# Kernel optimization log

Hardware: AMD Instinct MI355X
Metric: run time of the kernel (lower is better)

Reference implementation:

```python
import jax, jax.numpy as jnp
import numpy as np

H = 1024       # hidden_size
NH = 16        # num_heads
HD = H // NH   # head_dim
I = 4096       # intermediate_size
EPS = 1e-6


def setup_inputs() -> dict:
    key = jax.random.key(0)
    ks = jax.random.split(key, 10)
    s = 0.02
    return {
        "hidden_states": jax.random.normal(ks[0], (8, 1025, H), jnp.float32),
        "qkv_w": jax.random.normal(ks[1], (3 * H, H), jnp.float32) * s,
        "qkv_b": jnp.zeros((3 * H,), jnp.float32),
        "proj_w": jax.random.normal(ks[2], (H, H), jnp.float32) * s,
        "proj_b": jnp.zeros((H,), jnp.float32),
        "fc1_w": jax.random.normal(ks[3], (I, H), jnp.float32) * s,
        "fc1_b": jnp.zeros((I,), jnp.float32),
        "fc2_w": jax.random.normal(ks[4], (H, I), jnp.float32) * s,
        "fc2_b": jnp.zeros((H,), jnp.float32),
        "norm1_w": jnp.ones((H,), jnp.float32),
        "norm1_b": jnp.zeros((H,), jnp.float32),
        "norm2_w": jnp.ones((H,), jnp.float32),
        "norm2_b": jnp.zeros((H,), jnp.float32),
        "ls1": jnp.ones((H,), jnp.float32),
        "ls2": jnp.ones((H,), jnp.float32),
    }


def _layer_norm(x, w, b):
    mu = jnp.mean(x, axis=-1, keepdims=True)
    var = jnp.mean(jnp.square(x - mu), axis=-1, keepdims=True)
    return (x - mu) * jax.lax.rsqrt(var + EPS) * w + b


def _attention(x, qkv_w, qkv_b, proj_w, proj_b):
    B, N, _ = x.shape
    qkv = x @ qkv_w.T + qkv_b                       # [B,N,3H]
    qkv = qkv.reshape(B, N, 3, NH, HD)
    q, k, v = qkv[:, :, 0], qkv[:, :, 1], qkv[:, :, 2]  # [B,N,NH,HD]
    scale = HD ** -0.5
    scores = jnp.einsum("bqhd,bkhd->bhqk", q, k) * scale
    attn = jax.nn.softmax(scores, axis=-1)
    out = jnp.einsum("bhqk,bkhd->bqhd", attn, v).reshape(B, N, H)
    return out @ proj_w.T + proj_b


def _mlp(x, fc1_w, fc1_b, fc2_w, fc2_b):
    h = jax.nn.gelu(x @ fc1_w.T + fc1_b, approximate=False)
    return h @ fc2_w.T + fc2_b


def reference(hidden_states, qkv_w, qkv_b, proj_w, proj_b, fc1_w, fc1_b,
              fc2_w, fc2_b, norm1_w, norm1_b, norm2_w, norm2_b, ls1, ls2):
    x = hidden_states
    x = x + ls1 * _attention(_layer_norm(x, norm1_w, norm1_b),
                             qkv_w, qkv_b, proj_w, proj_b)
    x = x + ls2 * _mlp(_layer_norm(x, norm2_w, norm2_b),
                       fc1_w, fc1_b, fc2_w, fc2_b)
    return x
```

## Files before the change

### kernel.cpp

```cpp
#include <hip/hip_runtime.h>
#include <cstdint>
#include <cstddef>

typedef __bf16 bf16;
typedef __bf16 bf16x8 __attribute__((ext_vector_type(8)));
typedef __bf16 bf16x4 __attribute__((ext_vector_type(4)));
typedef float  floatx4 __attribute__((ext_vector_type(4)));

#define MFMA16(a,b,c) __builtin_amdgcn_mfma_f32_16x16x32_bf16((a),(b),(c),0,0,0)

__device__ __forceinline__ void async_copy16(void* lds, const void* g) {
    __builtin_amdgcn_global_load_lds(
        (const __attribute__((address_space(1))) unsigned int*)g,
        (__attribute__((address_space(3))) unsigned int*)lds,
        16, 0, 0);
}

__global__ __launch_bounds__(256) void cvt_all(const float* __restrict__ s0,
                                               const float* __restrict__ s1,
                                               const float* __restrict__ s2,
                                               const float* __restrict__ s3,
                                               bf16* __restrict__ d0,
                                               bf16* __restrict__ d1,
                                               bf16* __restrict__ d2,
                                               bf16* __restrict__ d3) {
    const int blk = blockIdx.x;
    const float* src; bf16* dst; int base;
    if (blk < 3072)      { src = s0; dst = d0; base = blk; }
    else if (blk < 4096) { src = s1; dst = d1; base = blk - 3072; }
    else if (blk < 8192) { src = s2; dst = d2; base = blk - 4096; }
    else                 { src = s3; dst = d3; base = blk - 8192; }
    const int i = base * 256 + threadIdx.x;
    const float4 v = ((const float4*)src)[i];
    bf16x4 o;
    o[0] = (bf16)v.x; o[1] = (bf16)v.y; o[2] = (bf16)v.z; o[3] = (bf16)v.w;
    ((bf16x4*)dst)[i] = o;
}

__global__ __launch_bounds__(256) void ln_kernel(const float* __restrict__ x,
                                                 const float* __restrict__ w,
                                                 const float* __restrict__ b,
                                                 bf16* __restrict__ out) {
    const int row = blockIdx.x;
    const int t = threadIdx.x;
    const float4 v = ((const float4*)(x + (size_t)row * 1024))[t];
    float s  = v.x + v.y + v.z + v.w;
    float ss = v.x*v.x + v.y*v.y + v.z*v.z + v.w*v.w;
#pragma unroll
    for (int m = 32; m >= 1; m >>= 1) {
        s  += __shfl_xor(s,  m, 64);
        ss += __shfl_xor(ss, m, 64);
    }
    __shared__ float red[8];
    const int wave = t >> 6, lane = t & 63;
    if (lane == 0) { red[wave] = s; red[4 + wave] = ss; }
    __syncthreads();
    s  = red[0] + red[1] + red[2] + red[3];
    ss = red[4] + red[5] + red[6] + red[7];
    const float mean = s * (1.0f / 1024.0f);
    const float var  = ss * (1.0f / 1024.0f) - mean * mean;
    const float inv  = rsqrtf(var + 1e-6f);
    const float4 wv = ((const float4*)w)[t];
    const float4 bv = ((const float4*)b)[t];
    bf16x4 o;
    o[0] = (bf16)((v.x - mean) * inv * wv.x + bv.x);
    o[1] = (bf16)((v.y - mean) * inv * wv.y + bv.y);
    o[2] = (bf16)((v.z - mean) * inv * wv.z + bv.z);
    o[3] = (bf16)((v.w - mean) * inv * wv.w + bv.w);
    *(bf16x4*)(out + (size_t)row * 1024 + t * 4) = o;
}

template <int EPI, bool MSTRIP>
__global__ __launch_bounds__(256, 4) void gemm_bt(
    const bf16* __restrict__ A, const bf16* __restrict__ B,
    const float* __restrict__ bias, void* __restrict__ Cout,
    const float* __restrict__ res, const float* __restrict__ lsv,
    int M, int N, int K, int mt_per) {
    __shared__ bf16 sA[2][4096];
    __shared__ bf16 sB[2][4096];
    const int tid  = threadIdx.x;
    const int wave = tid >> 6;
    const int lane = tid & 63;
    const int lrow = lane & 15;
    const int quad = lane >> 4;
    int m0, n0;
    if constexpr (MSTRIP) {
        const int mtile = blockIdx.x * mt_per + blockIdx.y % mt_per;
        const int ntile = blockIdx.y / mt_per;
        m0 = mtile * 128;
        n0 = ntile * 128;
        if (m0 >= M) return;
    } else {
        const int nx   = gridDim.x;
        const int lin  = blockIdx.y * nx + blockIdx.x;
        const int w    = nx >> 3;
        const int xcd  = lin & 7;
        const int slot = lin >> 3;
        const int ntile = xcd * w + (slot % w);
        const int mtile = slot / w;
        m0 = mtile * 128;
        n0 = ntile * 128;
    }
    const int wm = (wave >> 1) * 64;
    const int wn = (wave & 1) * 64;

    floatx4 acc[4][4] = {};

    const int part = tid & 3;
    int mA0 = m0 + 2 * (tid >> 3) + ((tid >> 2) & 1);
    int mA1 = mA0 + 64;
    if (mA0 > M - 1) mA0 = M - 1;
    if (mA1 > M - 1) mA1 = M - 1;
    const int nB0 = n0 + 2 * (tid >> 3) + ((tid >> 2) & 1);
    const bf16* AgC0 = A + (size_t)mA0 * K + part * 8;
    const bf16* AgC1 = A + (size_t)mA1 * K + part * 8;
    const bf16* BgC0 = B + (size_t)nB0 * K + part * 8;
    const bf16* BgC1 = B + (size_t)(nB0 + 64) * K + part * 8;
    const int ldsOff0 = wave * 512;
    const int ldsOff1 = 2048 + wave * 512;

    const int niter = K / 32;
    async_copy16(&sA[0][ldsOff0], AgC0);
    async_copy16(&sA[0][ldsOff1], AgC1);
    async_copy16(&sB[0][ldsOff0], BgC0);
    async_copy16(&sB[0][ldsOff1], BgC1);

    const int fbase = (lrow & 1) * 32 + quad * 8;
    int cur = 0;
    for (int it = 0; it < niter; ++it) {
        __syncthreads();
        if (it + 1 < niter) {
            const int kk = (it + 1) * 32;
            bf16* a = sA[cur ^ 1]; bf16* bb = sB[cur ^ 1];
            async_copy16(&a[ldsOff0],  AgC0 + kk);
            async_copy16(&a[ldsOff1],  AgC1 + kk);
            async_copy16(&bb[ldsOff0], BgC0 + kk);
            async_copy16(&bb[ldsOff1], BgC1 + kk);
        }
        const bf16* a = sA[cur]; const bf16* bb = sB[cur];
        bf16x8 af[4], bfr[4];
#pragma unroll
        for (int i = 0; i < 4; i++)
            af[i] = *(const bf16x8*)&a[((wm >> 1) + i * 8 + (lrow >> 1)) * 64 + fbase];
#pragma unroll
        for (int j = 0; j < 4; j++)
            bfr[j] = *(const bf16x8*)&bb[((wn >> 1) + j * 8 + (lrow >> 1)) * 64 + fbase];
#pragma unroll
        for (int i = 0; i < 4; i++)
#pragma unroll
            for (int j = 0; j < 4; j++)
                acc[i][j] = MFMA16(af[i], bfr[j], acc[i][j]);
        cur ^= 1;
    }

    const int nb = n0 + wn + lrow;
#pragma unroll
    for (int i = 0; i < 4; i++) {
        const int mb = m0 + wm + i * 16 + quad * 4;
#pragma unroll
        for (int r = 0; r < 4; r++) {
            const int m = mb + r;
            if (m < M) {
#pragma unroll
                for (int j = 0; j < 4; j++) {
                    const int n = nb + j * 16;
                    const float v = acc[i][j][r] + bias[n];
                    if constexpr (EPI == 0) {
                        ((bf16*)Cout)[(size_t)m * N + n] = (bf16)v;
                    } else if constexpr (EPI == 2) {
                        const float s_ = v * (0.7978845608f + 0.0356774081f * v * v);
                        const float e2s = __builtin_amdgcn_exp2f(2.8853900817779268f * s_);
                        const float g = v * (1.0f - __builtin_amdgcn_rcpf(1.0f + e2s));
                        ((bf16*)Cout)[(size_t)m * N + n] = (bf16)g;
                    } else {
                        ((float*)Cout)[(size_t)m * N + n] =
                            res[(size_t)m * N + n] + lsv[n] * v;
                    }
                }
            }
        }
    }
}

__global__ __launch_bounds__(256) void transpose_v(const bf16* __restrict__ qkv,
                                                   bf16* __restrict__ vt) {
    const int tt = blockIdx.x;
    const int bh = blockIdx.y;
    const int b = bh >> 4, h = bh & 15;
    __shared__ bf16 tile[64][72];
    const int t = threadIdx.x;
    const int tok0 = tt * 64;
#pragma unroll
    for (int i = 0; i < 4; i++) {
        const int idx4 = i * 256 + t;
        const int tl = idx4 >> 4;
        const int d4 = (idx4 & 15) * 4;
        const int tok = tok0 + tl;
        bf16x4 val;
        val[0] = (bf16)0.0f; val[1] = (bf16)0.0f; val[2] = (bf16)0.0f; val[3] = (bf16)0.0f;
        if (tok <= 1024) {
            val = *(const bf16x4*)(qkv + ((size_t)(b * 1025 + tok)) * 3072 + 2048 + h * 64 + d4);
        }
        tile[d4 + 0][tl] = val[0];
        tile[d4 + 1][tl] = val[1];
        tile[d4 + 2][tl] = val[2];
        tile[d4 + 3][tl] = val[3];
    }
    __syncthreads();
#pragma unroll
    for (int i = 0; i < 4; i++) {
        const int idx4 = i * 256 + t;
        const int d = idx4 >> 4;
        const int t4 = (idx4 & 15) * 4;
        bf16x4 o;
        o[0] = tile[d][t4 + 0]; o[1] = tile[d][t4 + 1];
        o[2] = tile[d][t4 + 2]; o[3] = tile[d][t4 + 3];
        *(bf16x4*)(vt + ((size_t)bh * 64 + d) * 1152 + tok0 + t4) = o;
    }
}

__global__ __launch_bounds__(256, 3) void attn_kernel(const bf16* __restrict__ qkv,
                                                      const bf16* __restrict__ vt,
                                                      bf16* __restrict__ o_out) {
    const int qt = blockIdx.x;
    const int bh = blockIdx.y;
    const int b = bh >> 4, h = bh & 15;
    __shared__ bf16 sK[2][4096];
    __shared__ bf16 sV[2][4096];
    __shared__ bf16 sQP[4608];
    const int tid = threadIdx.x, wave = tid >> 6, lane = tid & 63;
    const int lrow = lane & 15, quad = lane >> 4, lko = quad * 8;
    const float cexp = 0.18033688011112042f;
    const size_t row0 = (size_t)b * 1025;

#pragma unroll
    for (int i = 0; i < 2; i++) {
        const int g = i * 256 + tid;
        const int ks = g >> 8, rr = (g >> 2) & 63, p = g & 3;
        int qrow = qt * 64 + rr; if (qrow > 1024) qrow = 1024;
        async_copy16(&sQP[(i * 256 + wave * 64) * 8],
                     qkv + (row0 + qrow) * 3072 + h * 64 + ks * 32 + p * 8);
    }
    __syncthreads();
    bf16x8 qf[2];
    qf[0] = *(const bf16x8*)&sQP[(wave * 16 + lrow) * 32 + lko];
    qf[1] = *(const bf16x8*)&sQP[2048 + (wave * 16 + lrow) * 32 + lko];
#pragma unroll
    for (int i = 0; i < 8; i++) {
        qf[0][i] = (bf16)((float)qf[0][i] * cexp);
        qf[1][i] = (bf16)((float)qf[1][i] * cexp);
    }
    __syncthreads();

    const int kgs = tid >> 8, p_ = tid & 3;
    (void)kgs; (void)p_;

    {
#pragma unroll
        for (int i = 0; i < 2; i++) {
            const int g = i * 256 + tid;
            const int ks = g >> 8, tok = (g >> 2) & 63, p = g & 3;
            int krow = tok; if (krow > 1024) krow = 1024;
            async_copy16(&sK[0][(i * 256 + wave * 64) * 8],
                         qkv + (row0 + krow) * 3072 + 1024 + h * 64 + ks * 32 + p * 8);
        }
#pragma unroll
        for (int i = 0; i < 2; i++) {
            const int g = i * 256 + tid;
            const int kc = g >> 8, d = (g >> 2) & 63, p = g & 3;
            async_copy16(&sV[0][(i * 256 + wave * 64) * 8],
                         vt + ((size_t)bh * 64 + d) * 1152 + kc * 32 + p * 8);
        }
    }

    bf16x8 ones;
#pragma unroll
    for (int i = 0; i < 8; i++) ones[i] = (bf16)1.0f;

    floatx4 o[4] = {};
    floatx4 ol = {};
    bf16* pw = &sQP[wave * 1152];

    int cur = 0;
    for (int ktile = 0; ktile < 17; ++ktile) {
        const int kt0 = ktile * 64;
        __syncthreads();
        if (ktile < 16) {
            const int nt0 = kt0 + 64;
            bf16* kb = sK[cur ^ 1]; bf16* vb_ = sV[cur ^ 1];
#pragma unroll
            for (int i = 0; i < 2; i++) {
                const int g = i * 256 + tid;
                const int ks = g >> 8, tok = (g >> 2) & 63, p = g & 3;
                int krow = nt0 + tok; if (krow > 1024) krow = 1024;
                async_copy16(&kb[(i * 256 + wave * 64) * 8],
                             qkv + (row0 + krow) * 3072 + 1024 + h * 64 + ks * 32 + p * 8);
            }
#pragma unroll
            for (int i = 0; i < 2; i++) {
                const int g = i * 256 + tid;
                const int kc = g >> 8, d = (g >> 2) & 63, p = g & 3;
                async_copy16(&vb_[(i * 256 + wave * 64) * 8],
                             vt + ((size_t)bh * 64 + d) * 1152 + nt0 + kc * 32 + p * 8);
            }
        }
        const bf16* kbuf = sK[cur];
        const bf16* vbuf = sV[cur];

        const bool lastTile = (ktile == 16);
#pragma unroll
        for (int nt = 0; nt < 4; nt++) {
            bf16x8 k0 = *(const bf16x8*)&kbuf[(nt * 16 + lrow) * 32 + lko];
            bf16x8 k1 = *(const bf16x8*)&kbuf[2048 + (nt * 16 + lrow) * 32 + lko];
            floatx4 z = {};
            z = MFMA16(k0, qf[0], z);
            z = MFMA16(k1, qf[1], z);
            bf16x4 pb;
#pragma unroll
            for (int r = 0; r < 4; r++) {
                float p = __builtin_amdgcn_exp2f(z[r]);
                if (lastTile) {
                    const int ktok = kt0 + nt * 16 + quad * 4 + r;
                    p = (ktok <= 1024) ? p : 0.0f;
                }
                pb[r] = (bf16)p;
            }
            *(bf16x4*)&pw[lrow * 72 + nt * 16 + quad * 4] = pb;
        }
#pragma unroll
        for (int ks = 0; ks < 2; ks++) {
            bf16x8 pa = *(const bf16x8*)&pw[lrow * 72 + ks * 32 + lko];
#pragma unroll
            for (int j = 0; j < 4; j++) {
                bf16x8 vb = *(const bf16x8*)&vbuf[ks * 2048 + (j * 16 + lrow) * 32 + lko];
                o[j] = MFMA16(pa, vb, o[j]);
            }
            ol = MFMA16(pa, ones, ol);
        }
        cur ^= 1;
    }

#pragma unroll
    for (int r = 0; r < 4; r++) {
        const int q = qt * 64 + wave * 16 + quad * 4 + r;
        if (q <= 1024) {
            const float inv = 1.0f / ol[r];
            const size_t orow = (row0 + q) * 1024 + h * 64;
#pragma unroll
            for (int j = 0; j < 4; j++)
                o_out[orow + j * 16 + lrow] = (bf16)(o[j][r] * inv);
        }
    }
}

extern "C" void kernel_launch(void* const* d_in, const int* in_sizes, int n_in,
                              void* d_out, int out_size, void* d_ws, size_t ws_size,
                              hipStream_t stream) {
    const float* x      = (const float*)d_in[0];
    const float* qkv_w  = (const float*)d_in[1];
    const float* qkv_b  = (const float*)d_in[2];
    const float* proj_w = (const float*)d_in[3];
    const float* proj_b = (const float*)d_in[4];
    const float* fc1_w  = (const float*)d_in[5];
    const float* fc1_b  = (const float*)d_in[6];
    const float* fc2_w  = (const float*)d_in[7];
    const float* fc2_b  = (const float*)d_in[8];
    const float* n1w    = (const float*)d_in[9];
    const float* n1b    = (const float*)d_in[10];
    const float* n2w    = (const float*)d_in[11];
    const float* n2b    = (const float*)d_in[12];
    const float* ls1    = (const float*)d_in[13];
    const float* ls2    = (const float*)d_in[14];

    char* ws = (char*)d_ws;
    bf16*  wqkv  = (bf16*)(ws + 0);
    bf16*  wproj = (bf16*)(ws + 6291456);
    bf16*  wfc1  = (bf16*)(ws + 8388608);
    bf16*  wfc2  = (bf16*)(ws + 16777216);
    bf16*  vt    = (bf16*)(ws + 25165824);
    bf16*  attnO = (bf16*)(ws + 44040192);
    float* x1    = (float*)(ws + 60833792);
    bf16*  lnbuf = (bf16*)(ws + 94420992);
    bf16*  big   = (bf16*)(ws + 111214592);

    const int M = 8200;

    cvt_all<<<12288, 256, 0, stream>>>(qkv_w, proj_w, fc1_w, fc2_w,
                                       wqkv, wproj, wfc1, wfc2);

    ln_kernel<<<M, 256, 0, stream>>>(x, n1w, n1b, lnbuf);
    gemm_bt<0, false><<<dim3(24, 65), 256, 0, stream>>>(lnbuf, wqkv, qkv_b, (void*)big,
                                                        nullptr, nullptr, M, 3072, 1024, 0);
    transpose_v<<<dim3(17, 128), 256, 0, stream>>>(big, vt);
    attn_kernel<<<dim3(17, 128), 256, 0, stream>>>(big, vt, attnO);
    gemm_bt<1, true><<<dim3(8, 72), 256, 0, stream>>>(attnO, wproj, proj_b, (void*)x1,
                                                      x, ls1, M, 1024, 1024, 9);
    ln_kernel<<<M, 256, 0, stream>>>(x1, n2w, n2b, lnbuf);
    gemm_bt<2, false><<<dim3(32, 65), 256, 0, stream>>>(lnbuf, wfc1, fc1_b, (void*)big,
                                                        nullptr, nullptr, M, 4096, 1024, 0);
    gemm_bt<1, true><<<dim3(8, 72), 256, 0, stream>>>(big, wfc2, fc2_b, d_out,
                                                      x1, ls2, M, 1024, 4096, 9);
}
```

Before: 543.2 us.

## Swizzle LDS tile layout and hoist fragment loads ahead of async prefetch

Both the GEMM and the attention kernel now write their LDS tiles with an XOR swizzle on the 16-byte chunk index and read fragments with the matching swizzled offset, to reduce LDS bank conflicts on the bf16x8 fragment reads. The fragment loads from the current buffer are moved before the next tile's async global-to-LDS copies are issued. In attention, all K and V fragments are preloaded into registers, and the redundant barrier after the Q load is removed. The GEMM launch bound drops from 4 to 3 blocks per CU, giving more registers per thread at the cost of lower occupancy.

```diff
diff --git a/kernel.cpp b/kernel.cpp
--- a/kernel.cpp
+++ b/kernel.cpp
@@ -71,7 +71,7 @@
 }
 
 template <int EPI, bool MSTRIP>
-__global__ __launch_bounds__(256, 4) void gemm_bt(
+__global__ __launch_bounds__(256, 3) void gemm_bt(
     const bf16* __restrict__ A, const bf16* __restrict__ B,
     const float* __restrict__ bias, void* __restrict__ Cout,
     const float* __restrict__ res, const float* __restrict__ lsv,
@@ -106,45 +106,54 @@
 
     floatx4 acc[4][4] = {};
 
-    const int part = tid & 3;
-    int mA0 = m0 + 2 * (tid >> 3) + ((tid >> 2) & 1);
-    int mA1 = mA0 + 64;
-    if (mA0 > M - 1) mA0 = M - 1;
-    if (mA1 > M - 1) mA1 = M - 1;
-    const int nB0 = n0 + 2 * (tid >> 3) + ((tid >> 2) & 1);
-    const bf16* AgC0 = A + (size_t)mA0 * K + part * 8;
-    const bf16* AgC1 = A + (size_t)mA1 * K + part * 8;
-    const bf16* BgC0 = B + (size_t)nB0 * K + part * 8;
-    const bf16* BgC1 = B + (size_t)(nB0 + 64) * K + part * 8;
-    const int ldsOff0 = wave * 512;
-    const int ldsOff1 = 2048 + wave * 512;
+    const bf16* AgP[2];
+    const bf16* BgP[2];
+    int ldsb[2];
+#pragma unroll
+    for (int c = 0; c < 2; c++) {
+        const int g = c * 256 + tid;
+        const int r = g >> 3, p = g & 7;
+        const int l = p ^ (r & 7);
+        const int mr = 2 * r + (l >> 2);
+        const int kp = l & 3;
+        int am = m0 + mr; if (am > M - 1) am = M - 1;
+        AgP[c] = A + (size_t)am * K + kp * 8;
+        BgP[c] = B + (size_t)(n0 + mr) * K + kp * 8;
+        ldsb[c] = c * 2048 + wave * 512;
+    }
+
+    const int rbA  = (wm >> 1) + (lrow >> 1);
+    const int rbB  = (wn >> 1) + (lrow >> 1);
+    const int pswz = (((lrow & 1) * 4 + quad) ^ ((lrow >> 1) & 7)) * 8;
 
     const int niter = K / 32;
-    async_copy16(&sA[0][ldsOff0], AgC0);
-    async_copy16(&sA[0][ldsOff1], AgC1);
-    async_copy16(&sB[0][ldsOff0], BgC0);
-    async_copy16(&sB[0][ldsOff1], BgC1);
-
-    const int fbase = (lrow & 1) * 32 + quad * 8;
+#pragma unroll
+    for (int c = 0; c < 2; c++) {
+        async_copy16(&sA[0][ldsb[c]], AgP[c]);
+        async_copy16(&sB[0][ldsb[c]], BgP[c]);
+    }
+
     int cur = 0;
     for (int it = 0; it < niter; ++it) {
         __syncthreads();
+        const bf16* a  = sA[cur];
+        const bf16* bb = sB[cur];
+        bf16x8 af[4], bfr[4];
+#pragma unroll
+        for (int i = 0; i < 4; i++)
+            af[i] = *(const bf16x8*)&a[(rbA + i * 8) * 64 + pswz];
+#pragma unroll
+        for (int j = 0; j < 4; j++)
+            bfr[j] = *(const bf16x8*)&bb[(rbB + j * 8) * 64 + pswz];
         if (it + 1 < niter) {
             const int kk = (it + 1) * 32;
-            bf16* a = sA[cur ^ 1]; bf16* bb = sB[cur ^ 1];
-            async_copy16(&a[ldsOff0],  AgC0 + kk);
-            async_copy16(&a[ldsOff1],  AgC1 + kk);
-            async_copy16(&bb[ldsOff0], BgC0 + kk);
-            async_copy16(&bb[ldsOff1], BgC1 + kk);
-        }
-        const bf16* a = sA[cur]; const bf16* bb = sB[cur];
-        bf16x8 af[4], bfr[4];
-#pragma unroll
-        for (int i = 0; i < 4; i++)
-            af[i] = *(const bf16x8*)&a[((wm >> 1) + i * 8 + (lrow >> 1)) * 64 + fbase];
-#pragma unroll
-        for (int j = 0; j < 4; j++)
-            bfr[j] = *(const bf16x8*)&bb[((wn >> 1) + j * 8 + (lrow >> 1)) * 64 + fbase];
+            bf16* an = sA[cur ^ 1]; bf16* bn = sB[cur ^ 1];
+#pragma unroll
+            for (int c = 0; c < 2; c++) {
+                async_copy16(&an[ldsb[c]], AgP[c] + kk);
+                async_copy16(&bn[ldsb[c]], BgP[c] + kk);
+            }
+        }
 #pragma unroll
         for (int i = 0; i < 4; i++)
 #pragma unroll
@@ -250,27 +259,30 @@
         qf[0][i] = (bf16)((float)qf[0][i] * cexp);
         qf[1][i] = (bf16)((float)qf[1][i] * cexp);
     }
-    __syncthreads();
-
-    const int kgs = tid >> 8, p_ = tid & 3;
-    (void)kgs; (void)p_;
-
-    {
-#pragma unroll
-        for (int i = 0; i < 2; i++) {
-            const int g = i * 256 + tid;
-            const int ks = g >> 8, tok = (g >> 2) & 63, p = g & 3;
-            int krow = tok; if (krow > 1024) krow = 1024;
-            async_copy16(&sK[0][(i * 256 + wave * 64) * 8],
-                         qkv + (row0 + krow) * 3072 + 1024 + h * 64 + ks * 32 + p * 8);
-        }
-#pragma unroll
-        for (int i = 0; i < 2; i++) {
-            const int g = i * 256 + tid;
-            const int kc = g >> 8, d = (g >> 2) & 63, p = g & 3;
-            async_copy16(&sV[0][(i * 256 + wave * 64) * 8],
-                         vt + ((size_t)bh * 64 + d) * 1152 + kc * 32 + p * 8);
-        }
+
+    const bf16* KgP[2];
+    int kTok[2];
+    const bf16* VgP[2];
+    int ldsb[2];
+#pragma unroll
+    for (int c = 0; c < 2; c++) {
+        const int g = c * 256 + tid;
+        const int r = g >> 3, p = g & 7;
+        const int l = p ^ (r & 7);
+        const int L = 2 * r + (l >> 2);
+        const int kp = l & 3;
+        const int sub = L >> 6, idx = L & 63;
+        kTok[c] = idx;
+        KgP[c] = qkv + row0 * 3072 + 1024 + h * 64 + sub * 32 + kp * 8;
+        VgP[c] = vt + ((size_t)(bh * 64 + idx)) * 1152 + sub * 32 + kp * 8;
+        ldsb[c] = c * 2048 + wave * 512;
+    }
+
+#pragma unroll
+    for (int c = 0; c < 2; c++) {
+        int krow = kTok[c]; if (krow > 1024) krow = 1024;
+        async_copy16(&sK[0][ldsb[c]], KgP[c] + (size_t)krow * 3072);
+        async_copy16(&sV[0][ldsb[c]], VgP[c]);
     }
 
     bf16x8 ones;
@@ -280,41 +292,43 @@
     floatx4 o[4] = {};
     floatx4 ol = {};
     bf16* pw = &sQP[wave * 1152];
+    const int pswz = (((lrow & 1) * 4 + quad) ^ ((lrow >> 1) & 7)) * 8;
+    const int rb   = lrow >> 1;
 
     int cur = 0;
     for (int ktile = 0; ktile < 17; ++ktile) {
         const int kt0 = ktile * 64;
         __syncthreads();
+        const bf16* kbuf = sK[cur];
+        const bf16* vbuf = sV[cur];
+        bf16x8 kf[4][2], vf[2][4];
+#pragma unroll
+        for (int nt = 0; nt < 4; nt++)
+#pragma unroll
+            for (int ks = 0; ks < 2; ks++)
+                kf[nt][ks] = *(const bf16x8*)&kbuf[(ks * 32 + nt * 8 + rb) * 64 + pswz];
+#pragma unroll
+        for (int ks = 0; ks < 2; ks++)
+#pragma unroll
+            for (int j = 0; j < 4; j++)
+                vf[ks][j] = *(const bf16x8*)&vbuf[(ks * 32 + j * 8 + rb) * 64 + pswz];
         if (ktile < 16) {
             const int nt0 = kt0 + 64;
             bf16* kb = sK[cur ^ 1]; bf16* vb_ = sV[cur ^ 1];
 #pragma unroll
-            for (int i = 0; i < 2; i++) {
-                const int g = i * 256 + tid;
-                const int ks = g >> 8, tok = (g >> 2) & 63, p = g & 3;
-                int krow = nt0 + tok; if (krow > 1024) krow = 1024;
-                async_copy16(&kb[(i * 256 + wave * 64) * 8],
-                             qkv + (row0 + krow) * 3072 + 1024 + h * 64 + ks * 32 + p * 8);
+            for (int c = 0; c < 2; c++) {
+                int krow = nt0 + kTok[c]; if (krow > 1024) krow = 1024;
+                async_copy16(&kb[ldsb[c]], KgP[c] + (size_t)krow * 3072);
+                async_copy16(&vb_[ldsb[c]], VgP[c] + nt0);
             }
-#pragma unroll
-            for (int i = 0; i < 2; i++) {
-                const int g = i * 256 + tid;
-                const int kc = g >> 8, d = (g >> 2) & 63, p = g & 3;
-                async_copy16(&vb_[(i * 256 + wave * 64) * 8],
-                             vt + ((size_t)bh * 64 + d) * 1152 + nt0 + kc * 32 + p * 8);
-            }
-        }
-        const bf16* kbuf = sK[cur];
-        const bf16* vbuf = sV[cur];
+        }
 
         const bool lastTile = (ktile == 16);
 #pragma unroll
         for (int nt = 0; nt < 4; nt++) {
-            bf16x8 k0 = *(const bf16x8*)&kbuf[(nt * 16 + lrow) * 32 + lko];
-            bf16x8 k1 = *(const bf16x8*)&kbuf[2048 + (nt * 16 + lrow) * 32 + lko];
             floatx4 z = {};
-            z = MFMA16(k0, qf[0], z);
-            z = MFMA16(k1, qf[1], z);
+            z = MFMA16(kf[nt][0], qf[0], z);
+            z = MFMA16(kf[nt][1], qf[1], z);
             bf16x4 pb;
 #pragma unroll
             for (int r = 0; r < 4; r++) {
@@ -331,10 +345,8 @@
         for (int ks = 0; ks < 2; ks++) {
             bf16x8 pa = *(const bf16x8*)&pw[lrow * 72 + ks * 32 + lko];
 #pragma unroll
-            for (int j = 0; j < 4; j++) {
-                bf16x8 vb = *(const bf16x8*)&vbuf[ks * 2048 + (j * 16 + lrow) * 32 + lko];
-                o[j] = MFMA16(pa, vb, o[j]);
-            }
+            for (int j = 0; j < 4; j++)
+                o[j] = MFMA16(pa, vf[ks][j], o[j]);
             ol = MFMA16(pa, ones, ol);
         }
         cur ^= 1;
```

Measured after the change: 509.3 us. -6.2%, faster.
